# Kernel tuning notes

Measured on AMD Instinct MI355X. Metric: run time of the kernel, lower is better.

The kernel has to match this reference:

```python
import jax, jax.numpy as jnp
import numpy as np

OBS, H, F1, A, T, B = 128, 128, 256, 18, 128, 1024


def _ln(x, w, b, eps=1e-5):
    mu = jnp.mean(x, -1, keepdims=True)
    xc = x - mu
    var = jnp.mean(xc * xc, -1, keepdims=True)
    return xc * jax.lax.rsqrt(var + eps) * w + b


def _features(x, w1, b1, w2, b2, lnw, lnb):
    h = jax.nn.relu(x @ w1.T + b1)      # [N, 256]
    h = h @ w2.T + b2                   # [N, 128]
    return jax.nn.relu(_ln(h, lnw, lnb))


def _masked_lstm(xs, ds, h0, c0, wih, whh, b):
    # xs: [T,B,H], ds: [T,B] float; PyTorch gate order i,f,g,o
    def step(carry, inp):
        h, c = carry
        xt, dt = inp
        m = (1.0 - dt)[:, None]
        h = h * m
        c = c * m
        g = xt @ wih.T + h @ whh.T + b  # [B, 4H]
        i, f, gg, o = jnp.split(g, 4, axis=-1)
        c = jax.nn.sigmoid(f) * c + jax.nn.sigmoid(i) * jnp.tanh(gg)
        h = jax.nn.sigmoid(o) * jnp.tanh(c)
        return (h, c), h
    (hT, cT), hs = jax.lax.scan(step, (h0, c0), (xs, ds))
    return hs, hT, cT


def setup_inputs() -> dict:
    key = jax.random.key(0)
    ks = iter(jax.random.split(key, 64))
    p = lambda shape, s=0.05: jax.random.normal(next(ks), shape, jnp.float32) * s
    inp = {
        'x': jax.random.normal(next(ks), (T * B, OBS), jnp.float32),
        'actor_h': jnp.zeros((1, B, H), jnp.float32),
        'actor_c': jnp.zeros((1, B, H), jnp.float32),
        'critic_h': jnp.zeros((1, B, H), jnp.float32),
        'critic_c': jnp.zeros((1, B, H), jnp.float32),
        'done': jax.random.randint(next(ks), (T * B,), 0, 2, jnp.int32),
        'action': jax.random.randint(next(ks), (T * B,), 0, A, jnp.int64),
        # actor params
        'af_w1': p((F1, OBS)), 'af_b1': p((F1,)),
        'af_w2': p((H, F1)), 'af_b2': p((H,)),
        'af_lnw': jnp.ones((H,), jnp.float32), 'af_lnb': jnp.zeros((H,), jnp.float32),
        'a_wih': p((4 * H, H)), 'a_whh': p((4 * H, H)), 'a_b': p((4 * H,)),
        'a_lnw': jnp.ones((H,), jnp.float32), 'a_lnb': jnp.zeros((H,), jnp.float32),
        'a_hw': p((A, H)), 'a_hb': p((A,)),
        # critic params
        'cf_w1': p((F1, OBS)), 'cf_b1': p((F1,)),
        'cf_w2': p((H, F1)), 'cf_b2': p((H,)),
        'cf_lnw': jnp.ones((H,), jnp.float32), 'cf_lnb': jnp.zeros((H,), jnp.float32),
        'c_wih': p((4 * H, H)), 'c_whh': p((4 * H, H)), 'c_b': p((4 * H,)),
        'c_lnw': jnp.ones((H,), jnp.float32), 'c_lnb': jnp.zeros((H,), jnp.float32),
        'c_hw': p((1, H)), 'c_hb': p((1,)),
    }
    return inp


def reference(x, actor_h, actor_c, critic_h, critic_c,
              af_w1, af_b1, af_w2, af_b2, af_lnw, af_lnb,
              a_wih, a_whh, a_b, a_lnw, a_lnb, a_hw, a_hb,
              cf_w1, cf_b1, cf_w2, cf_b2, cf_lnw, cf_lnb,
              c_wih, c_whh, c_b, c_lnw, c_lnb, c_hw, c_hb,
              done, action):
    bsz = actor_h.shape[1]
    ds = done.astype(jnp.float32).reshape(-1, bsz)  # [T, B]

    # actor branch
    af = _features(x, af_w1, af_b1, af_w2, af_b2, af_lnw, af_lnb).reshape(-1, bsz, H)
    hs, ahT, acT = _masked_lstm(af, ds, actor_h[0], actor_c[0], a_wih, a_whh, a_b)
    ah = _ln(hs.reshape(-1, H), a_lnw, a_lnb)
    logits = ah @ a_hw.T + a_hb                     # [N, A]
    logp_all = jax.nn.log_softmax(logits)
    logp = jnp.take_along_axis(logp_all, action[:, None], axis=1)[:, 0]
    entropy = -jnp.sum(jnp.exp(logp_all) * logp_all, axis=-1)

    # critic branch
    cf = _features(x, cf_w1, cf_b1, cf_w2, cf_b2, cf_lnw, cf_lnb).reshape(-1, bsz, H)
    cs, chT, ccT = _masked_lstm(cf, ds, critic_h[0], critic_c[0], c_wih, c_whh, c_b)
    ch = _ln(cs.reshape(-1, H), c_lnw, c_lnb)
    value = ch @ c_hw.T + c_hb                      # [N, 1]

    return (action, logp, entropy, value,
            ahT[None], acT[None], chT[None], ccT[None])
```

## Files before the change

kernel.cpp:

```cpp
#include <hip/hip_runtime.h>
#include <stdint.h>
#include <stddef.h>

#define OBS 128
#define F1D 256
#define HD  128
#define NA  18
#define TT  128
#define BB  1024
#define NN  (TT*BB)
#define LOG2E 1.442695041f

typedef __attribute__((ext_vector_type(8))) short short8;
typedef __attribute__((ext_vector_type(4))) float f32x4;

__device__ __forceinline__ unsigned short f2bf(float f) {
  union { float f; uint32_t u; } v; v.f = f;
  uint32_t u = v.u;
  u += 0x7fffu + ((u >> 16) & 1u);
  return (unsigned short)(u >> 16);
}
__device__ __forceinline__ float bf2f(uint32_t hu) {
  union { uint32_t u; float f; } v; v.u = hu << 16;
  return v.f;
}
__device__ __forceinline__ f32x4 mfma16(short8 a, short8 b, f32x4 c) {
  return __builtin_amdgcn_mfma_f32_16x16x32_bf16(a, b, c, 0, 0, 0);
}
__device__ __forceinline__ short8 cvt8(const float* p, float sc) {
  float4 a = *(const float4*)p;
  float4 b = *(const float4*)(p + 4);
  union { unsigned short u[8]; short8 s; } o;
  o.u[0]=f2bf(a.x*sc); o.u[1]=f2bf(a.y*sc); o.u[2]=f2bf(a.z*sc); o.u[3]=f2bf(a.w*sc);
  o.u[4]=f2bf(b.x*sc); o.u[5]=f2bf(b.y*sc); o.u[6]=f2bf(b.z*sc); o.u[7]=f2bf(b.w*sc);
  return o.s;
}
__device__ __forceinline__ short8 pin(short8 v) {
  int4 i = *(int4*)&v;
  asm volatile("" : "+v"(i.x), "+v"(i.y), "+v"(i.z), "+v"(i.w));
  return *(short8*)&i;
}

__global__ __launch_bounds__(512, 2) void fused_kernel(
    const float* __restrict__ x, const int* __restrict__ done,
    const int* __restrict__ action,
    const float* __restrict__ aw1, const float* __restrict__ ab1,
    const float* __restrict__ aw2, const float* __restrict__ ab2,
    const float* __restrict__ aflnw, const float* __restrict__ aflnb,
    const float* __restrict__ awih, const float* __restrict__ awhh,
    const float* __restrict__ a_b,
    const float* __restrict__ alnw, const float* __restrict__ alnb,
    const float* __restrict__ ahw, const float* __restrict__ ahb,
    const float* __restrict__ cw1, const float* __restrict__ cb1,
    const float* __restrict__ cw2, const float* __restrict__ cb2,
    const float* __restrict__ cflnw, const float* __restrict__ cflnb,
    const float* __restrict__ cwih, const float* __restrict__ cwhh,
    const float* __restrict__ c_b,
    const float* __restrict__ clnw, const float* __restrict__ clnb,
    const float* __restrict__ chw, const float* __restrict__ chb,
    const float* __restrict__ ah0, const float* __restrict__ ac0,
    const float* __restrict__ ch0, const float* __restrict__ cc0,
    unsigned short* __restrict__ featg, float* __restrict__ dout)
{
  int g = blockIdx.x;
  int br = g >> 7;
  int chunk = g & 127;
  int base8 = chunk * 8;

  const float* w1  = br ? cw1 : aw1;
  const float* b1  = br ? cb1 : ab1;
  const float* w2  = br ? cw2 : aw2;
  const float* b2  = br ? cb2 : ab2;
  const float* flw = br ? cflnw : aflnw;
  const float* flb = br ? cflnb : aflnb;
  const float* wih = br ? cwih : awih;
  const float* whh = br ? cwhh : awhh;
  const float* gb  = br ? c_b : a_b;
  const float* h0  = br ? ch0 : ah0;
  const float* c0  = br ? cc0 : ac0;
  unsigned short* feat = featg + (size_t)br * NN * HD;

  __shared__ unsigned short xs[2][32*OBS];
  __shared__ unsigned short h1s[2][32*F1D];
  __shared__ float lnsum[2][32*8];
  __shared__ float mls[(TT+1)*8];
  __shared__ unsigned short hlds[2][8*128];
  __shared__ float hwl[NA*HD];
  __shared__ float pa[HD], pb[HD], pc[HD];
  __shared__ float hbl[NA];
  __shared__ int flagS;

  int tid = threadIdx.x;
  int w = tid >> 6, lane = tid & 63, q = lane >> 4, ln = lane & 15;
  int team = tid >> 8, t_tid = tid & 255, w4 = w & 3;

  {
    short8 b1f[4][4]; float b1v[4];
    #pragma unroll
    for (int ct = 0; ct < 4; ++ct) {
      int nn = w4*64 + ct*16 + ln;
      b1v[ct] = b1[nn];
      #pragma unroll
      for (int kf = 0; kf < 4; ++kf)
        b1f[ct][kf] = pin(cvt8(&w1[nn*OBS + kf*32 + q*8], 1.0f));
    }
    short8 b2f[2][8]; float b2v[2], lwv[2], lbv[2];
    #pragma unroll
    for (int nt = 0; nt < 2; ++nt) {
      int nn = w4*32 + nt*16 + ln;
      b2v[nt] = b2[nn]; lwv[nt] = flw[nn]; lbv[nt] = flb[nn];
      #pragma unroll
      for (int kf = 0; kf < 8; ++kf)
        b2f[nt][kf] = pin(cvt8(&w2[nn*F1D + kf*32 + q*8], 1.0f));
    }
    float4 xr[4];
    #pragma unroll
    for (int s = 0; s < 4; ++s) {
      int e4 = t_tid + s*256;
      int r = e4 >> 5, c4 = e4 & 31;
      size_t grow = (size_t)(team*4 + (r>>3))*BB + base8 + (r&7);
      xr[s] = ((const float4*)x)[grow*32 + c4];
    }
    for (int j = 0; j < 16; ++j) {
      int jj = j*2 + team;
      #pragma unroll
      for (int s = 0; s < 4; ++s) {
        int e = (t_tid + s*256) * 4;
        int r = e >> 7, k = e & 127;
        int ad = r*128 + ((((k>>3) ^ (r&15)) << 3)) + (k&7);
        uint2 d;
        d.x = (uint32_t)f2bf(xr[s].x) | ((uint32_t)f2bf(xr[s].y) << 16);
        d.y = (uint32_t)f2bf(xr[s].z) | ((uint32_t)f2bf(xr[s].w) << 16);
        *(uint2*)&xs[team][ad] = d;
      }
      __syncthreads();
      {
        int jjn = (j < 15) ? jj + 2 : jj;
        #pragma unroll
        for (int s = 0; s < 4; ++s) {
          int e4 = t_tid + s*256;
          int r = e4 >> 5, c4 = e4 & 31;
          size_t grow = (size_t)(jjn*4 + (r>>3))*BB + base8 + (r&7);
          xr[s] = ((const float4*)x)[grow*32 + c4];
        }
      }
      short8 af[2][4];
      #pragma unroll
      for (int mt = 0; mt < 2; ++mt)
        #pragma unroll
        for (int kf = 0; kf < 4; ++kf)
          af[mt][kf] = *(const short8*)&xs[team][(mt*16 + ln)*128 + ((((kf<<2)|q) ^ ln) << 3)];
      #pragma unroll
      for (int ct = 0; ct < 4; ++ct) {
        int nn = w4*64 + ct*16 + ln;
        #pragma unroll
        for (int mt = 0; mt < 2; ++mt) {
          f32x4 acc = {b1v[ct], b1v[ct], b1v[ct], b1v[ct]};
          #pragma unroll
          for (int kf = 0; kf < 4; ++kf) acc = mfma16(af[mt][kf], b1f[ct][kf], acc);
          #pragma unroll
          for (int rg = 0; rg < 4; ++rg) {
            float v = acc[rg] > 0.0f ? acc[rg] : 0.0f;
            int rrow = mt*16 + q*4 + rg;
            h1s[team][rrow*256 + (((nn>>3) ^ (rrow&15)) << 3) + (nn&7)] = f2bf(v);
          }
        }
      }
      __syncthreads();
      f32x4 acc2[2][2];
      #pragma unroll
      for (int mt = 0; mt < 2; ++mt) {
        short8 ah[8];
        #pragma unroll
        for (int kf = 0; kf < 8; ++kf)
          ah[kf] = *(const short8*)&h1s[team][(mt*16 + ln)*256 + ((((kf<<2)|q) ^ ln) << 3)];
        #pragma unroll
        for (int nt = 0; nt < 2; ++nt) {
          f32x4 acc = {b2v[nt], b2v[nt], b2v[nt], b2v[nt]};
          #pragma unroll
          for (int kf = 0; kf < 8; ++kf) acc = mfma16(ah[kf], b2f[nt][kf], acc);
          acc2[nt][mt] = acc;
        }
      }
      #pragma unroll
      for (int mt = 0; mt < 2; ++mt)
        #pragma unroll
        for (int rg = 0; rg < 4; ++rg) {
          float v0 = acc2[0][mt][rg], v1 = acc2[1][mt][rg];
          float s = v0 + v1, ssq = v0*v0 + v1*v1;
          #pragma unroll
          for (int m = 1; m < 16; m <<= 1) { s += __shfl_xor(s, m); ssq += __shfl_xor(ssq, m); }
          if (ln == 0) {
            int r = mt*16 + q*4 + rg;
            lnsum[team][r*8 + w4*2]     = s;
            lnsum[team][r*8 + w4*2 + 1] = ssq;
          }
        }
      __syncthreads();
      #pragma unroll
      for (int mt = 0; mt < 2; ++mt)
        #pragma unroll
        for (int rg = 0; rg < 4; ++rg) {
          int r = mt*16 + q*4 + rg;
          float4 p0 = *(const float4*)&lnsum[team][r*8];
          float4 p1 = *(const float4*)&lnsum[team][r*8 + 4];
          float S  = p0.x + p0.z + p1.x + p1.z;
          float SS = p0.y + p0.w + p1.y + p1.w;
          float mu = S * (1.0f/128.0f);
          float var = SS * (1.0f/128.0f) - mu*mu;
          float rstd = rsqrtf(var + 1e-5f);
          size_t grow = (size_t)(jj*4 + (r>>3))*BB + base8 + (r&7);
          #pragma unroll
          for (int nt = 0; nt < 2; ++nt) {
            float t = (acc2[nt][mt][rg] - mu) * rstd * lwv[nt] + lbv[nt];
            if (t < 0.0f) t = 0.0f;
            feat[grow*HD + w4*32 + nt*16 + ln] = f2bf(t);
          }
        }
      __syncthreads();
    }
  }

  int n = w*16 + ln;
  short8 bfr[4][8]; float bias[4];
  #pragma unroll
  for (int g4 = 0; g4 < 4; ++g4) {
    int gn = g4*128 + n;
    float sc = (g4 == 2) ? -2.0f*LOG2E : -LOG2E;
    bias[g4] = gb[gn] * sc;
    #pragma unroll
    for (int kf = 0; kf < 8; ++kf) {
      const float* src = (kf < 4) ? &wih[gn*HD + kf*32 + q*8]
                                  : &whh[gn*HD + (kf-4)*32 + q*8];
      bfr[g4][kf] = pin(cvt8(src, sc));
    }
  }
  for (int i = tid; i < (TT+1)*8; i += 512)
    mls[i] = (i < TT*8) ? 1.0f - (float)done[(i>>3)*BB + base8 + (i&7)] : 1.0f;

  const int loff = (base8 + (ln>>1))*HD + q*8;
  int soff[2], hoffw[2], haddr[4];
  #pragma unroll
  for (int j = 0; j < 2; ++j) {
    int r = q*2 + j;
    soff[j]  = (base8 + r)*HD + n;
    hoffw[j] = r*128 + (((n>>3) ^ r) << 3) + (n&7);
  }
  #pragma unroll
  for (int kf = 0; kf < 4; ++kf) {
    int rr = ln >> 1;
    haddr[kf] = rr*128 + ((((kf<<2)|q) ^ rr) << 3);
  }
  float hp[2], cp[2]; unsigned short hu_prev[2];
  #pragma unroll
  for (int j = 0; j < 2; ++j) {
    int b = base8 + q*2 + j;
    hp[j] = h0[b*HD + n];
    cp[j] = c0[b*HD + n];
    hu_prev[j] = 0;
  }
  short8 afr[4], nfr[4];
  #pragma unroll
  for (int kf = 0; kf < 4; ++kf)
    afr[kf] = *(const short8*)&feat[loff + kf*32];
  __syncthreads();
  #pragma unroll
  for (int j = 0; j < 2; ++j) {
    float m = mls[q*2 + j];
    cp[j] *= m;
    hlds[0][hoffw[j]] = f2bf(hp[j] * m);
  }
  __syncthreads();

#define LSTM_STEP(TTT, CUR, NXT, HB)                                           \
  {                                                                            \
    short8 hfr[4];                                                             \
    _Pragma("unroll")                                                          \
    for (int kf = 0; kf < 4; ++kf)                                             \
      hfr[kf] = *(const short8*)&hlds[HB][haddr[kf]];                          \
    {                                                                          \
      int tp = (TTT) > 0 ? (TTT) - 1 : 0;                                      \
      unsigned short* sq = feat + (size_t)tp * (BB*HD);                        \
      sq[soff[0]] = hu_prev[0];                                                \
      sq[soff[1]] = hu_prev[1];                                                \
    }                                                                          \
    int tn = ((TTT) + 1 < TT) ? (TTT) + 1 : TT - 1;                            \
    const unsigned short* fq = feat + (size_t)tn * (BB*HD);                    \
    _Pragma("unroll")                                                          \
    for (int kf = 0; kf < 4; ++kf)                                             \
      NXT[kf] = *(const short8*)&fq[loff + kf*32];                             \
    f32x4 a0 = {bias[0],bias[0],bias[0],bias[0]};                              \
    f32x4 a1 = {bias[1],bias[1],bias[1],bias[1]};                              \
    f32x4 a2 = {bias[2],bias[2],bias[2],bias[2]};                              \
    f32x4 a3 = {bias[3],bias[3],bias[3],bias[3]};                              \
    _Pragma("unroll")                                                          \
    for (int kf = 0; kf < 4; ++kf) {                                           \
      a0 = mfma16(CUR[kf], bfr[0][kf], a0);                                    \
      a1 = mfma16(CUR[kf], bfr[1][kf], a1);                                    \
      a2 = mfma16(CUR[kf], bfr[2][kf], a2);                                    \
      a3 = mfma16(CUR[kf], bfr[3][kf], a3);                                    \
    }                                                                          \
    _Pragma("unroll")                                                          \
    for (int kf = 0; kf < 4; ++kf) {                                           \
      a0 = mfma16(hfr[kf], bfr[0][4+kf], a0);                                  \
      a1 = mfma16(hfr[kf], bfr[1][4+kf], a1);                                  \
      a2 = mfma16(hfr[kf], bfr[2][4+kf], a2);                                  \
      a3 = mfma16(hfr[kf], bfr[3][4+kf], a3);                                  \
    }                                                                          \
    float2 mn = *(const float2*)&mls[((TTT)+1)*8 + q*2];                       \
    _Pragma("unroll")                                                          \
    for (int j = 0; j < 2; ++j) {                                              \
      int rg = j*2;     \
      float si = __builtin_amdgcn_rcpf(1.0f + __builtin_amdgcn_exp2f(a0[rg])); \
      float sf = __builtin_amdgcn_rcpf(1.0f + __builtin_amdgcn_exp2f(a1[rg])); \
      float tg = __builtin_fmaf(2.0f,                                          \
                   __builtin_amdgcn_rcpf(1.0f + __builtin_amdgcn_exp2f(a2[rg])), -1.0f); \
      float so = __builtin_amdgcn_rcpf(1.0f + __builtin_amdgcn_exp2f(a3[rg])); \
      float cn = __builtin_fmaf(sf, cp[j], si*tg);                             \
      float th = __builtin_fmaf(2.0f,                                          \
                   __builtin_amdgcn_rcpf(1.0f + __builtin_amdgcn_exp2f(-2.0f*LOG2E*cn)), -1.0f); \
      float hn = so * th;                                                      \
      unsigned short hu = f2bf(hn);                                            \
      hu_prev[j] = hu;                                                         \
      bool live = ((&mn.x)[j] != 0.0f);                                        \
      cp[j] = live ? cn : 0.0f;                                                \
      hp[j] = hn;                                                              \
      hlds[(HB)^1][hoffw[j]] = live ? hu : (unsigned short)0;                  \
    }                                                                          \
    __syncthreads();                                                           \
  }

  for (int t = 0; t < TT; t += 2) {
    LSTM_STEP(t,   afr, nfr, 0)
    LSTM_STEP(t+1, nfr, afr, 1)
  }
#undef LSTM_STEP

  {
    unsigned short* sq = feat + (size_t)(TT-1)*(BB*HD);
    sq[soff[0]] = hu_prev[0];
    sq[soff[1]] = hu_prev[1];
  }
  {
    float* outh = dout + (size_t)(4 + br*2) * NN;
    float* outc = dout + (size_t)(5 + br*2) * NN;
    #pragma unroll
    for (int j = 0; j < 2; ++j) {
      int b = base8 + q*2 + j;
      outh[b*HD + n] = hp[j];
      outc[b*HD + n] = cp[j];
    }
  }

  if (tid == 0) flagS = 0;
  int localf = 0;
  if (br == 0) {
    for (int i = tid; i < NA*HD; i += 512) hwl[i] = ahw[i];
    if (tid < NA) hbl[tid] = ahb[tid];
    if (tid < HD) { pa[tid] = alnw[tid]; pb[tid] = alnb[tid]; }
    for (int i = 2*tid + 1; i < 4096; i += 1024) localf |= action[i];
  } else {
    if (tid < HD) { pa[tid] = clnw[tid]; pb[tid] = clnb[tid]; pc[tid] = chw[tid]; }
    if (tid == 0) hbl[0] = chb[0];
  }
  __syncthreads();
  if (localf) flagS = 1;
  __syncthreads();

  if (br == 0) {
    int fl = flagS;
    for (int kk = 0; kk < 2; ++kk) {
      int k = tid + kk*512;
      int rr = (k >> 3)*BB + base8 + (k & 7);
      int act = fl ? action[rr] : (int)(((const long long*)action)[rr]);
      dout[rr] = (float)act;
      if (act < 0) act = 0;
      if (act > NA-1) act = NA-1;
      uint32_t hw_[64];
      const uint32_t* hp2 = (const uint32_t*)(feat + (size_t)rr*HD);
      for (int i = 0; i < 16; ++i) *(uint4*)&hw_[i*4] = ((const uint4*)hp2)[i];
      float s = 0.0f, ss = 0.0f;
      for (int i = 0; i < 64; ++i) {
        float f0 = bf2f(hw_[i] & 0xffffu), f1 = bf2f(hw_[i] >> 16);
        s += f0 + f1; ss += f0*f0 + f1*f1;
      }
      float mu = s * (1.0f/128.0f);
      float var = ss * (1.0f/128.0f) - mu*mu;
      float rstd = rsqrtf(var + 1e-5f);
      float lg[NA];
      for (int a = 0; a < NA; ++a) lg[a] = hbl[a];
      for (int i = 0; i < 64; ++i) {
        int k0 = i*2;
        float f0 = (bf2f(hw_[i] & 0xffffu) - mu)*rstd*pa[k0]   + pb[k0];
        float f1 = (bf2f(hw_[i] >> 16)     - mu)*rstd*pa[k0+1] + pb[k0+1];
        for (int a = 0; a < NA; ++a)
          lg[a] += f0*hwl[a*HD + k0] + f1*hwl[a*HD + k0 + 1];
      }
      float mx = lg[0];
      for (int a = 1; a < NA; ++a) mx = fmaxf(mx, lg[a]);
      float se = 0.0f;
      for (int a = 0; a < NA; ++a) se += __expf(lg[a] - mx);
      float lse = __logf(se);
      dout[(size_t)NN + rr] = lg[act] - mx - lse;
      float ent = 0.0f;
      for (int a = 0; a < NA; ++a) { float lp = lg[a] - mx - lse; ent -= __expf(lp)*lp; }
      dout[(size_t)2*NN + rr] = ent;
    }
  } else {
    for (int kk = 0; kk < 2; ++kk) {
      int k = tid + kk*512;
      int rr = (k >> 3)*BB + base8 + (k & 7);
      uint32_t hw_[64];
      const uint32_t* hp2 = (const uint32_t*)(feat + (size_t)rr*HD);
      for (int i = 0; i < 16; ++i) *(uint4*)&hw_[i*4] = ((const uint4*)hp2)[i];
      float s = 0.0f, ss = 0.0f;
      for (int i = 0; i < 64; ++i) {
        float f0 = bf2f(hw_[i] & 0xffffu), f1 = bf2f(hw_[i] >> 16);
        s += f0 + f1; ss += f0*f0 + f1*f1;
      }
      float mu = s * (1.0f/128.0f);
      float var = ss * (1.0f/128.0f) - mu*mu;
      float rstd = rsqrtf(var + 1e-5f);
      float v = hbl[0];
      for (int i = 0; i < 64; ++i) {
        int k0 = i*2;
        float f0 = (bf2f(hw_[i] & 0xffffu) - mu)*rstd*pa[k0]   + pb[k0];
        float f1 = (bf2f(hw_[i] >> 16)     - mu)*rstd*pa[k0+1] + pb[k0+1];
        v += f0*pc[k0] + f1*pc[k0+1];
      }
      dout[(size_t)3*NN + rr] = v;
    }
  }
}

extern "C" void kernel_launch(void* const* d_in, const int* in_sizes, int n_in,
                              void* d_out, int out_size, void* d_ws, size_t ws_size,
                              hipStream_t stream) {
  (void)in_sizes; (void)n_in; (void)out_size; (void)ws_size;
  const float* x    = (const float*)d_in[0];
  const float* ah0  = (const float*)d_in[1];
  const float* ac0  = (const float*)d_in[2];
  const float* ch0  = (const float*)d_in[3];
  const float* cc0  = (const float*)d_in[4];
  const int*   done = (const int*)d_in[5];
  const int*   act  = (const int*)d_in[6];
  const float* aw1  = (const float*)d_in[7];
  const float* ab1  = (const float*)d_in[8];
  const float* aw2  = (const float*)d_in[9];
  const float* ab2  = (const float*)d_in[10];
  const float* aflnw= (const float*)d_in[11];
  const float* aflnb= (const float*)d_in[12];
  const float* awih = (const float*)d_in[13];
  const float* awhh = (const float*)d_in[14];
  const float* a_b  = (const float*)d_in[15];
  const float* alnw = (const float*)d_in[16];
  const float* alnb = (const float*)d_in[17];
  const float* ahw  = (const float*)d_in[18];
  const float* ahb  = (const float*)d_in[19];
  const float* cw1  = (const float*)d_in[20];
  const float* cb1  = (const float*)d_in[21];
  const float* cw2  = (const float*)d_in[22];
  const float* cb2  = (const float*)d_in[23];
  const float* cflnw= (const float*)d_in[24];
  const float* cflnb= (const float*)d_in[25];
  const float* cwih = (const float*)d_in[26];
  const float* cwhh = (const float*)d_in[27];
  const float* c_b  = (const float*)d_in[28];
  const float* clnw = (const float*)d_in[29];
  const float* clnb = (const float*)d_in[30];
  const float* chw  = (const float*)d_in[31];
  const float* chb  = (const float*)d_in[32];

  unsigned short* featb = (unsigned short*)d_ws;
  float* out = (float*)d_out;

  fused_kernel<<<256, 512, 0, stream>>>(
      x, done, act,
      aw1, ab1, aw2, ab2, aflnw, aflnb, awih, awhh, a_b, alnw, alnb, ahw, ahb,
      cw1, cb1, cw2, cb2, cflnw, cflnb, cwih, cwhh, c_b, clnw, clnb, chw, chb,
      ah0, ac0, ch0, cc0,
      featb, out);
}
```

Measured before the change: 446.4 us.

## Compute actor head logits with MFMA and split row LayerNorm across four threads

The post-LSTM epilogue previously had each thread handle one full row: a serial 128-wide LayerNorm and an 18x128 scalar dot product against shared-memory weights. Now four threads share each row, with shuffles for the statistics. The normalized rows are staged as bf16 in shared memory, and the actor head logits are computed with MFMA against zero-padded weight fragments held in registers. The critic value head is also split across four threads with a shuffle reduction, and the feature-stage shared buffers are unioned into one region for reuse. This cuts scalar FMA and serial work in the tail phase, at the cost of bf16 rounding of the normalized activations and extra block barriers.

```diff
diff --git a/kernel.cpp b/kernel.cpp
--- a/kernel.cpp
+++ b/kernel.cpp
@@ -80,14 +80,12 @@
   const float* c0  = br ? cc0 : ac0;
   unsigned short* feat = featg + (size_t)br * NN * HD;
 
-  __shared__ unsigned short xs[2][32*OBS];
-  __shared__ unsigned short h1s[2][32*F1D];
-  __shared__ float lnsum[2][32*8];
+  __shared__ __align__(16) char smemA[51200];
   __shared__ float mls[(TT+1)*8];
   __shared__ unsigned short hlds[2][8*128];
-  __shared__ float hwl[NA*HD];
-  __shared__ float pa[HD], pb[HD], pc[HD];
+  __shared__ float pa[HD], pb[HD], cws[HD];
   __shared__ float hbl[NA];
+  __shared__ float cbsS;
   __shared__ int flagS;
 
   int tid = threadIdx.x;
@@ -95,6 +93,10 @@
   int team = tid >> 8, t_tid = tid & 255, w4 = w & 3;
 
   {
+    unsigned short* xst  = (unsigned short*)smemA + team*4096;
+    unsigned short* h1st = (unsigned short*)(smemA + 16384) + team*8192;
+    float*          lnst = (float*)(smemA + 49152) + team*256;
+
     short8 b1f[4][4]; float b1v[4];
     #pragma unroll
     for (int ct = 0; ct < 4; ++ct) {
@@ -131,7 +133,7 @@
         uint2 d;
         d.x = (uint32_t)f2bf(xr[s].x) | ((uint32_t)f2bf(xr[s].y) << 16);
         d.y = (uint32_t)f2bf(xr[s].z) | ((uint32_t)f2bf(xr[s].w) << 16);
-        *(uint2*)&xs[team][ad] = d;
+        *(uint2*)&xst[ad] = d;
       }
       __syncthreads();
       {
@@ -149,7 +151,7 @@
       for (int mt = 0; mt < 2; ++mt)
         #pragma unroll
         for (int kf = 0; kf < 4; ++kf)
-          af[mt][kf] = *(const short8*)&xs[team][(mt*16 + ln)*128 + ((((kf<<2)|q) ^ ln) << 3)];
+          af[mt][kf] = *(const short8*)&xst[(mt*16 + ln)*128 + ((((kf<<2)|q) ^ ln) << 3)];
       #pragma unroll
       for (int ct = 0; ct < 4; ++ct) {
         int nn = w4*64 + ct*16 + ln;
@@ -162,7 +164,7 @@
           for (int rg = 0; rg < 4; ++rg) {
             float v = acc[rg] > 0.0f ? acc[rg] : 0.0f;
             int rrow = mt*16 + q*4 + rg;
-            h1s[team][rrow*256 + (((nn>>3) ^ (rrow&15)) << 3) + (nn&7)] = f2bf(v);
+            h1st[rrow*256 + (((nn>>3) ^ (rrow&15)) << 3) + (nn&7)] = f2bf(v);
           }
         }
       }
@@ -173,7 +175,7 @@
         short8 ah[8];
         #pragma unroll
         for (int kf = 0; kf < 8; ++kf)
-          ah[kf] = *(const short8*)&h1s[team][(mt*16 + ln)*256 + ((((kf<<2)|q) ^ ln) << 3)];
+          ah[kf] = *(const short8*)&h1st[(mt*16 + ln)*256 + ((((kf<<2)|q) ^ ln) << 3)];
         #pragma unroll
         for (int nt = 0; nt < 2; ++nt) {
           f32x4 acc = {b2v[nt], b2v[nt], b2v[nt], b2v[nt]};
@@ -186,14 +188,14 @@
       for (int mt = 0; mt < 2; ++mt)
         #pragma unroll
         for (int rg = 0; rg < 4; ++rg) {
-          float v0 = acc2[0][mt][rg], v1 = acc2[1][mt][rg];
-          float s = v0 + v1, ssq = v0*v0 + v1*v1;
+          float s = acc2[0][mt][rg] + acc2[1][mt][rg];
+          float ssq = acc2[0][mt][rg]*acc2[0][mt][rg] + acc2[1][mt][rg]*acc2[1][mt][rg];
           #pragma unroll
           for (int m = 1; m < 16; m <<= 1) { s += __shfl_xor(s, m); ssq += __shfl_xor(ssq, m); }
           if (ln == 0) {
             int r = mt*16 + q*4 + rg;
-            lnsum[team][r*8 + w4*2]     = s;
-            lnsum[team][r*8 + w4*2 + 1] = ssq;
+            lnst[r*8 + w4*2]     = s;
+            lnst[r*8 + w4*2 + 1] = ssq;
           }
         }
       __syncthreads();
@@ -202,8 +204,8 @@
         #pragma unroll
         for (int rg = 0; rg < 4; ++rg) {
           int r = mt*16 + q*4 + rg;
-          float4 p0 = *(const float4*)&lnsum[team][r*8];
-          float4 p1 = *(const float4*)&lnsum[team][r*8 + 4];
+          float4 p0 = *(const float4*)&lnst[r*8];
+          float4 p1 = *(const float4*)&lnst[r*8 + 4];
           float S  = p0.x + p0.z + p1.x + p1.z;
           float SS = p0.y + p0.w + p1.y + p1.w;
           float mu = S * (1.0f/128.0f);
@@ -222,55 +224,56 @@
   }
 
   int n = w*16 + ln;
-  short8 bfr[4][8]; float bias[4];
-  #pragma unroll
-  for (int g4 = 0; g4 < 4; ++g4) {
-    int gn = g4*128 + n;
-    float sc = (g4 == 2) ? -2.0f*LOG2E : -LOG2E;
-    bias[g4] = gb[gn] * sc;
-    #pragma unroll
-    for (int kf = 0; kf < 8; ++kf) {
-      const float* src = (kf < 4) ? &wih[gn*HD + kf*32 + q*8]
-                                  : &whh[gn*HD + (kf-4)*32 + q*8];
-      bfr[g4][kf] = pin(cvt8(src, sc));
-    }
-  }
-  for (int i = tid; i < (TT+1)*8; i += 512)
-    mls[i] = (i < TT*8) ? 1.0f - (float)done[(i>>3)*BB + base8 + (i&7)] : 1.0f;
-
-  const int loff = (base8 + (ln>>1))*HD + q*8;
-  int soff[2], hoffw[2], haddr[4];
-  #pragma unroll
-  for (int j = 0; j < 2; ++j) {
-    int r = q*2 + j;
-    soff[j]  = (base8 + r)*HD + n;
-    hoffw[j] = r*128 + (((n>>3) ^ r) << 3) + (n&7);
-  }
-  #pragma unroll
-  for (int kf = 0; kf < 4; ++kf) {
-    int rr = ln >> 1;
-    haddr[kf] = rr*128 + ((((kf<<2)|q) ^ rr) << 3);
-  }
-  float hp[2], cp[2]; unsigned short hu_prev[2];
-  #pragma unroll
-  for (int j = 0; j < 2; ++j) {
-    int b = base8 + q*2 + j;
-    hp[j] = h0[b*HD + n];
-    cp[j] = c0[b*HD + n];
-    hu_prev[j] = 0;
-  }
-  short8 afr[4], nfr[4];
-  #pragma unroll
-  for (int kf = 0; kf < 4; ++kf)
-    afr[kf] = *(const short8*)&feat[loff + kf*32];
-  __syncthreads();
-  #pragma unroll
-  for (int j = 0; j < 2; ++j) {
-    float m = mls[q*2 + j];
-    cp[j] *= m;
-    hlds[0][hoffw[j]] = f2bf(hp[j] * m);
-  }
-  __syncthreads();
+  {
+    short8 bfr[4][8]; float bias[4];
+    #pragma unroll
+    for (int g4 = 0; g4 < 4; ++g4) {
+      int gn = g4*128 + n;
+      float sc = (g4 == 2) ? -2.0f*LOG2E : -LOG2E;
+      bias[g4] = gb[gn] * sc;
+      #pragma unroll
+      for (int kf = 0; kf < 8; ++kf) {
+        const float* src = (kf < 4) ? &wih[gn*HD + kf*32 + q*8]
+                                    : &whh[gn*HD + (kf-4)*32 + q*8];
+        bfr[g4][kf] = pin(cvt8(src, sc));
+      }
+    }
+    for (int i = tid; i < (TT+1)*8; i += 512)
+      mls[i] = (i < TT*8) ? 1.0f - (float)done[(i>>3)*BB + base8 + (i&7)] : 1.0f;
+
+    const int loff = (base8 + (ln>>1))*HD + q*8;
+    int soff[2], hoffw[2], haddr[4];
+    #pragma unroll
+    for (int j = 0; j < 2; ++j) {
+      int r = q*2 + j;
+      soff[j]  = (base8 + r)*HD + n;
+      hoffw[j] = r*128 + (((n>>3) ^ r) << 3) + (n&7);
+    }
+    #pragma unroll
+    for (int kf = 0; kf < 4; ++kf) {
+      int rr = ln >> 1;
+      haddr[kf] = rr*128 + ((((kf<<2)|q) ^ rr) << 3);
+    }
+    float hp[2], cp[2]; unsigned short hu_prev[2];
+    #pragma unroll
+    for (int j = 0; j < 2; ++j) {
+      int b = base8 + q*2 + j;
+      hp[j] = h0[b*HD + n];
+      cp[j] = c0[b*HD + n];
+      hu_prev[j] = 0;
+    }
+    short8 afr[4], nfr[4];
+    #pragma unroll
+    for (int kf = 0; kf < 4; ++kf)
+      afr[kf] = *(const short8*)&feat[loff + kf*32];
+    __syncthreads();
+    #pragma unroll
+    for (int j = 0; j < 2; ++j) {
+      float m = mls[q*2 + j];
+      cp[j] *= m;
+      hlds[0][hoffw[j]] = f2bf(hp[j] * m);
+    }
+    __syncthreads();
 
 #define LSTM_STEP(TTT, CUR, NXT, HB)                                           \
   {                                                                            \
@@ -330,105 +333,173 @@
     __syncthreads();                                                           \
   }
 
-  for (int t = 0; t < TT; t += 2) {
-    LSTM_STEP(t,   afr, nfr, 0)
-    LSTM_STEP(t+1, nfr, afr, 1)
+    for (int t = 0; t < TT; t += 2) {
+      LSTM_STEP(t,   afr, nfr, 0)
+      LSTM_STEP(t+1, nfr, afr, 1)
+    }
+#undef LSTM_STEP
+
+    {
+      unsigned short* sq = feat + (size_t)(TT-1)*(BB*HD);
+      sq[soff[0]] = hu_prev[0];
+      sq[soff[1]] = hu_prev[1];
+    }
+    {
+      float* outh = dout + (size_t)(4 + br*2) * NN;
+      float* outc = dout + (size_t)(5 + br*2) * NN;
+      #pragma unroll
+      for (int j = 0; j < 2; ++j) {
+        int b = base8 + q*2 + j;
+        outh[b*HD + n] = hp[j];
+        outc[b*HD + n] = cp[j];
+      }
+    }
   }
-#undef LSTM_STEP
-
-  {
-    unsigned short* sq = feat + (size_t)(TT-1)*(BB*HD);
-    sq[soff[0]] = hu_prev[0];
-    sq[soff[1]] = hu_prev[1];
+
+  if (tid == 0) flagS = 0;
+  if (tid < HD) {
+    pa[tid] = br ? clnw[tid] : alnw[tid];
+    pb[tid] = br ? clnb[tid] : alnb[tid];
+    if (br) cws[tid] = chw[tid];
   }
-  {
-    float* outh = dout + (size_t)(4 + br*2) * NN;
-    float* outc = dout + (size_t)(5 + br*2) * NN;
-    #pragma unroll
-    for (int j = 0; j < 2; ++j) {
-      int b = base8 + q*2 + j;
-      outh[b*HD + n] = hp[j];
-      outc[b*HD + n] = cp[j];
-    }
-  }
-
-  if (tid == 0) flagS = 0;
   int localf = 0;
   if (br == 0) {
-    for (int i = tid; i < NA*HD; i += 512) hwl[i] = ahw[i];
     if (tid < NA) hbl[tid] = ahb[tid];
-    if (tid < HD) { pa[tid] = alnw[tid]; pb[tid] = alnb[tid]; }
     for (int i = 2*tid + 1; i < 4096; i += 1024) localf |= action[i];
-  } else {
-    if (tid < HD) { pa[tid] = clnw[tid]; pb[tid] = clnb[tid]; pc[tid] = chw[tid]; }
-    if (tid == 0) hbl[0] = chb[0];
-  }
+  } else if (tid == 0) cbsS = chb[0];
   __syncthreads();
   if (localf) flagS = 1;
   __syncthreads();
 
+  int sub = tid & 3, kidx = tid >> 2;
   if (br == 0) {
+    unsigned short* hsn = (unsigned short*)smemA;
+    float* co = (float*)(smemA + 32768);
+    short8 hbf[2][4];
+    #pragma unroll
+    for (int nt = 0; nt < 2; ++nt) {
+      int nn = nt*16 + ln;
+      #pragma unroll
+      for (int kf = 0; kf < 4; ++kf) {
+        short8 z = {0,0,0,0,0,0,0,0};
+        hbf[nt][kf] = (nn < NA) ? pin(cvt8(&ahw[nn*HD + kf*32 + q*8], 1.0f)) : z;
+      }
+    }
     int fl = flagS;
-    for (int kk = 0; kk < 2; ++kk) {
-      int k = tid + kk*512;
-      int rr = (k >> 3)*BB + base8 + (k & 7);
-      int act = fl ? action[rr] : (int)(((const long long*)action)[rr]);
-      dout[rr] = (float)act;
-      if (act < 0) act = 0;
-      if (act > NA-1) act = NA-1;
-      uint32_t hw_[64];
-      const uint32_t* hp2 = (const uint32_t*)(feat + (size_t)rr*HD);
-      for (int i = 0; i < 16; ++i) *(uint4*)&hw_[i*4] = ((const uint4*)hp2)[i];
-      float s = 0.0f, ss = 0.0f;
-      for (int i = 0; i < 64; ++i) {
-        float f0 = bf2f(hw_[i] & 0xffffu), f1 = bf2f(hw_[i] >> 16);
-        s += f0 + f1; ss += f0*f0 + f1*f1;
-      }
+    for (int ch = 0; ch < 8; ++ch) {
+      {
+        int k = ch*128 + kidx;
+        int rrow = (k >> 3)*BB + base8 + (k & 7);
+        const unsigned short* hp2 = feat + (size_t)rrow*HD + sub*32;
+        uint4 d0 = *(const uint4*)hp2;
+        uint4 d1 = *(const uint4*)(hp2 + 8);
+        uint4 d2 = *(const uint4*)(hp2 + 16);
+        uint4 d3 = *(const uint4*)(hp2 + 24);
+        float nv[32];
+        #define UP(W_, B_) { nv[B_] = bf2f((W_) & 0xffffu); nv[(B_)+1] = bf2f((W_) >> 16); }
+        UP(d0.x,0) UP(d0.y,2) UP(d0.z,4) UP(d0.w,6)
+        UP(d1.x,8) UP(d1.y,10) UP(d1.z,12) UP(d1.w,14)
+        UP(d2.x,16) UP(d2.y,18) UP(d2.z,20) UP(d2.w,22)
+        UP(d3.x,24) UP(d3.y,26) UP(d3.z,28) UP(d3.w,30)
+        #undef UP
+        float s = 0.0f, ssq = 0.0f;
+        #pragma unroll
+        for (int j = 0; j < 32; ++j) { s += nv[j]; ssq += nv[j]*nv[j]; }
+        s += __shfl_xor(s, 1); ssq += __shfl_xor(ssq, 1);
+        s += __shfl_xor(s, 2); ssq += __shfl_xor(ssq, 2);
+        float mu = s * (1.0f/128.0f);
+        float var = ssq * (1.0f/128.0f) - mu*mu;
+        float rstd = rsqrtf(var + 1e-5f);
+        #pragma unroll
+        for (int cc = 0; cc < 4; ++cc) {
+          unsigned short ob[8];
+          #pragma unroll
+          for (int j = 0; j < 8; ++j) {
+            int c = sub*32 + cc*8 + j;
+            ob[j] = f2bf((nv[cc*8+j] - mu) * rstd * pa[c] + pb[c]);
+          }
+          int c8 = sub*4 + cc;
+          *(short8*)&hsn[kidx*128 + ((c8 ^ (kidx & 15)) << 3)] = *(short8*)ob;
+        }
+      }
+      __syncthreads();
+      {
+        short8 afh[4];
+        #pragma unroll
+        for (int kf = 0; kf < 4; ++kf)
+          afh[kf] = *(const short8*)&hsn[(w*16 + ln)*128 + ((((kf<<2)|q) ^ ln) << 3)];
+        #pragma unroll
+        for (int nt = 0; nt < 2; ++nt) {
+          f32x4 acc = {0.0f, 0.0f, 0.0f, 0.0f};
+          #pragma unroll
+          for (int kf = 0; kf < 4; ++kf) acc = mfma16(afh[kf], hbf[nt][kf], acc);
+          #pragma unroll
+          for (int rg = 0; rg < 4; ++rg)
+            co[(w*16 + q*4 + rg)*36 + nt*16 + ln] = acc[rg];
+        }
+      }
+      __syncthreads();
+      if (tid < 128) {
+        int k = ch*128 + tid;
+        int rrow = (k >> 3)*BB + base8 + (k & 7);
+        int act = fl ? action[rrow] : (int)(((const long long*)action)[rrow]);
+        dout[rrow] = (float)act;
+        int aidx = act < 0 ? 0 : (act > NA-1 ? NA-1 : act);
+        float lg[NA];
+        #pragma unroll
+        for (int a = 0; a < NA; ++a) lg[a] = co[tid*36 + a] + hbl[a];
+        float mx = lg[0];
+        #pragma unroll
+        for (int a = 1; a < NA; ++a) mx = fmaxf(mx, lg[a]);
+        float se = 0.0f;
+        #pragma unroll
+        for (int a = 0; a < NA; ++a) se += __expf(lg[a] - mx);
+        float lse = __logf(se);
+        float lpa = 0.0f, ent = 0.0f;
+        #pragma unroll
+        for (int a = 0; a < NA; ++a) {
+          float lp = lg[a] - mx - lse;
+          ent -= __expf(lp) * lp;
+          lpa += (a == aidx) ? lp : 0.0f;
+        }
+        dout[(size_t)NN + rrow] = lpa;
+        dout[(size_t)2*NN + rrow] = ent;
+      }
+      __syncthreads();
+    }
+  } else {
+    for (int ch = 0; ch < 8; ++ch) {
+      int k = ch*128 + kidx;
+      int rrow = (k >> 3)*BB + base8 + (k & 7);
+      const unsigned short* hp2 = feat + (size_t)rrow*HD + sub*32;
+      uint4 d0 = *(const uint4*)hp2;
+      uint4 d1 = *(const uint4*)(hp2 + 8);
+      uint4 d2 = *(const uint4*)(hp2 + 16);
+      uint4 d3 = *(const uint4*)(hp2 + 24);
+      float nv[32];
+      #define UP(W_, B_) { nv[B_] = bf2f((W_) & 0xffffu); nv[(B_)+1] = bf2f((W_) >> 16); }
+      UP(d0.x,0) UP(d0.y,2) UP(d0.z,4) UP(d0.w,6)
+      UP(d1.x,8) UP(d1.y,10) UP(d1.z,12) UP(d1.w,14)
+      UP(d2.x,16) UP(d2.y,18) UP(d2.z,20) UP(d2.w,22)
+      UP(d3.x,24) UP(d3.y,26) UP(d3.z,28) UP(d3.w,30)
+      #undef UP
+      float s = 0.0f, ssq = 0.0f;
+      #pragma unroll
+      for (int j = 0; j < 32; ++j) { s += nv[j]; ssq += nv[j]*nv[j]; }
+      s += __shfl_xor(s, 1); ssq += __shfl_xor(ssq, 1);
+      s += __shfl_xor(s, 2); ssq += __shfl_xor(ssq, 2);
       float mu = s * (1.0f/128.0f);
-      float var = ss * (1.0f/128.0f) - mu*mu;
+      float var = ssq * (1.0f/128.0f) - mu*mu;
       float rstd = rsqrtf(var + 1e-5f);
-      float lg[NA];
-      for (int a = 0; a < NA; ++a) lg[a] = hbl[a];
-      for (int i = 0; i < 64; ++i) {
-        int k0 = i*2;
-        float f0 = (bf2f(hw_[i] & 0xffffu) - mu)*rstd*pa[k0]   + pb[k0];
-        float f1 = (bf2f(hw_[i] >> 16)     - mu)*rstd*pa[k0+1] + pb[k0+1];
-        for (int a = 0; a < NA; ++a)
-          lg[a] += f0*hwl[a*HD + k0] + f1*hwl[a*HD + k0 + 1];
-      }
-      float mx = lg[0];
-      for (int a = 1; a < NA; ++a) mx = fmaxf(mx, lg[a]);
-      float se = 0.0f;
-      for (int a = 0; a < NA; ++a) se += __expf(lg[a] - mx);
-      float lse = __logf(se);
-      dout[(size_t)NN + rr] = lg[act] - mx - lse;
-      float ent = 0.0f;
-      for (int a = 0; a < NA; ++a) { float lp = lg[a] - mx - lse; ent -= __expf(lp)*lp; }
-      dout[(size_t)2*NN + rr] = ent;
-    }
-  } else {
-    for (int kk = 0; kk < 2; ++kk) {
-      int k = tid + kk*512;
-      int rr = (k >> 3)*BB + base8 + (k & 7);
-      uint32_t hw_[64];
-      const uint32_t* hp2 = (const uint32_t*)(feat + (size_t)rr*HD);
-      for (int i = 0; i < 16; ++i) *(uint4*)&hw_[i*4] = ((const uint4*)hp2)[i];
-      float s = 0.0f, ss = 0.0f;
-      for (int i = 0; i < 64; ++i) {
-        float f0 = bf2f(hw_[i] & 0xffffu), f1 = bf2f(hw_[i] >> 16);
-        s += f0 + f1; ss += f0*f0 + f1*f1;
-      }
-      float mu = s * (1.0f/128.0f);
-      float var = ss * (1.0f/128.0f) - mu*mu;
-      float rstd = rsqrtf(var + 1e-5f);
-      float v = hbl[0];
-      for (int i = 0; i < 64; ++i) {
-        int k0 = i*2;
-        float f0 = (bf2f(hw_[i] & 0xffffu) - mu)*rstd*pa[k0]   + pb[k0];
-        float f1 = (bf2f(hw_[i] >> 16)     - mu)*rstd*pa[k0+1] + pb[k0+1];
-        v += f0*pc[k0] + f1*pc[k0+1];
-      }
-      dout[(size_t)3*NN + rr] = v;
+      float dot = 0.0f;
+      #pragma unroll
+      for (int j = 0; j < 32; ++j) {
+        int c = sub*32 + j;
+        dot += ((nv[j] - mu) * rstd * pa[c] + pb[c]) * cws[c];
+      }
+      dot += __shfl_xor(dot, 1);
+      dot += __shfl_xor(dot, 2);
+      if (sub == 0) dout[(size_t)3*NN + rrow] = dot + cbsS;
     }
   }
 }
```

Result: faster. 413.6 us (-7.3%).
